# Optimization experiments

Hardware: AMD Instinct MI355X
Metric: run time of the kernel (lower is better)

The kernel has to match this reference:

```python
import jax, jax.numpy as jnp
import numpy as np

IMG = 800.0
OUT_H = OUT_W = 7
SR = 2  # sampling_ratio
SCALES = (0.25, 0.125, 0.0625, 0.03125)
CANON_SCALE = 224.0
CANON_LVL = 4.0
K_MIN, K_MAX = 2, 5


def _make_boxes(key, n):
    k1, k2, k3 = jax.random.split(key, 3)
    c = jax.random.uniform(k1, (n, 2), minval=0.0, maxval=IMG)          # centers (cx, cy)
    logs = jax.random.uniform(k2, (n, 2), minval=np.log(32.0), maxval=np.log(512.0))
    wh = jnp.exp(logs)                                                   # sizes 32..512 px
    x1y1 = jnp.clip(c - wh / 2, 0.0, IMG - 2.0)
    x2y2 = jnp.clip(c + wh / 2, x1y1 + 1.0, IMG)
    return jnp.concatenate([x1y1, x2y2], axis=1)  # [n,4] xyxy


def setup_inputs() -> dict:
    key = jax.random.key(0)
    ks = jax.random.split(key, 6)
    return {
        "feat0": jax.random.normal(ks[0], (2, 256, 200, 200), jnp.float32),
        "feat1": jax.random.normal(ks[1], (2, 256, 100, 100), jnp.float32),
        "feat2": jax.random.normal(ks[2], (2, 256, 50, 50), jnp.float32),
        "feat3": jax.random.normal(ks[3], (2, 256, 25, 25), jnp.float32),
        "boxes0": _make_boxes(ks[4], 256),
        "boxes1": _make_boxes(ks[5], 256),
    }


def _roi_align(feat_bhwc, rois, scale):
    """torchvision roi_align (aligned=False). feat_bhwc: [B,H,W,C], rois: [R,5] (b,x1,y1,x2,y2)."""
    B, H, W, C = feat_bhwc.shape
    R = rois.shape[0]
    bidx = rois[:, 0].astype(jnp.int32)
    x1, y1, x2, y2 = (rois[:, i] * scale for i in (1, 2, 3, 4))
    roi_w = jnp.maximum(x2 - x1, 1.0)
    roi_h = jnp.maximum(y2 - y1, 1.0)
    bin_w = roi_w / OUT_W
    bin_h = roi_h / OUT_H
    # sample grid: (g + 0.5)/SR bins == bin_index + (sub + 0.5)/SR
    gy = (jnp.arange(OUT_H * SR, dtype=feat_bhwc.dtype) + 0.5) / SR
    gx = (jnp.arange(OUT_W * SR, dtype=feat_bhwc.dtype) + 0.5) / SR
    y = y1[:, None] + gy[None, :] * bin_h[:, None]  # [R, GY]
    x = x1[:, None] + gx[None, :] * bin_w[:, None]  # [R, GX]

    def prep(c, size):
        valid = ((c > -1.0) & (c < size)).astype(feat_bhwc.dtype)
        c = jnp.clip(c, 0.0)
        lo = jnp.minimum(jnp.floor(c).astype(jnp.int32), size - 1)
        hi = jnp.minimum(lo + 1, size - 1)
        frac = jnp.where(lo >= size - 1, 0.0, c - lo.astype(feat_bhwc.dtype))
        return lo, hi, frac, valid

    yl, yh, fy, vy = prep(y, H)
    xl, xh, fx, vx = prep(x, W)
    b = bidx[:, None, None]

    def g(yi, xi):  # gather -> [R, GY, GX, C]
        return feat_bhwc[b, yi[:, :, None], xi[:, None, :]]

    wy = fy[:, :, None, None]
    wx = fx[:, None, :, None]
    val = (g(yl, xl) * (1 - wy) * (1 - wx) + g(yl, xh) * (1 - wy) * wx
           + g(yh, xl) * wy * (1 - wx) + g(yh, xh) * wy * wx)
    val = val * (vy[:, :, None, None] * vx[:, None, :, None])
    val = val.reshape(R, OUT_H, SR, OUT_W, SR, C).mean(axis=(2, 4))  # avg over SRxSR samples
    return jnp.transpose(val, (0, 3, 1, 2))  # [R, C, OUT_H, OUT_W]


def _forward(feat0, feat1, feat2, feat3, boxes0, boxes1):
    feats = [feat0, feat1, feat2, feat3]
    boxes = [boxes0, boxes1]
    # convert_to_roi_format
    ids = jnp.concatenate([jnp.full((b.shape[0], 1), i, dtype=b.dtype) for i, b in enumerate(boxes)], 0)
    cat = jnp.concatenate(boxes, 0)  # [R,4]
    rois = jnp.concatenate([ids, cat], 1)  # [R,5]
    # LevelMapper (FPN eq. 1)
    area = (cat[:, 2] - cat[:, 0]) * (cat[:, 3] - cat[:, 1])
    s = jnp.sqrt(area)
    tgt = jnp.floor(CANON_LVL + jnp.log2(s / CANON_SCALE) + 1e-6)
    levels = (jnp.clip(tgt, K_MIN, K_MAX) - K_MIN).astype(jnp.int32)  # [R] in 0..3
    per = [_roi_align(jnp.transpose(f, (0, 2, 3, 1)), rois, sc) for f, sc in zip(feats, SCALES)]
    stacked = jnp.stack(per)  # [L, R, C, 7, 7]
    R = rois.shape[0]
    return stacked[levels, jnp.arange(R)]  # route each roi to its level


def reference(feat0, feat1, feat2, feat3, boxes0, boxes1):
    return _forward(feat0, feat1, feat2, feat3, boxes0, boxes1)
```

## Files before the change

kernel.cpp:

```cpp
#include <hip/hip_runtime.h>


#define OUT_HW 7
#define NBINS 49
#define NCH 256
#define RPB 256

__global__ __launch_bounds__(256) void msroi_kernel(
    const float* __restrict__ f0, const float* __restrict__ f1,
    const float* __restrict__ f2, const float* __restrict__ f3,
    const float* __restrict__ boxes0, const float* __restrict__ boxes1,
    float* __restrict__ out)
{
    __shared__ float lds_out[NCH * NBINS];

    const int r    = blockIdx.x;
    const int tid  = threadIdx.x;
    const int lane = tid & 63;
    const int wid  = tid >> 6;

    const int b = (r < RPB) ? 0 : 1;
    const float* bx = (b == 0) ? (boxes0 + (size_t)r * 4)
                               : (boxes1 + (size_t)(r - RPB) * 4);
    const float x1b = bx[0], y1b = bx[1], x2b = bx[2], y2b = bx[3];

    const float area = (x2b - x1b) * (y2b - y1b);
    const float s    = sqrtf(area);
    const float tgt  = floorf(4.0f + log2f(s / 224.0f) + 1e-6f);
    const float lvlf = fminf(fmaxf(tgt, 2.0f), 5.0f);
    const int   lvl  = (int)lvlf - 2;

    int H, W;
    const float* feat;
    float scale;
    switch (lvl) {
      case 0:  feat = f0; H = 200; W = 200; scale = 0.25f;    break;
      case 1:  feat = f1; H = 100; W = 100; scale = 0.125f;   break;
      case 2:  feat = f2; H = 50;  W = 50;  scale = 0.0625f;  break;
      default: feat = f3; H = 25;  W = 25;  scale = 0.03125f; break;
    }
    const int HW = H * W;

    const float x1 = x1b * scale, y1 = y1b * scale;
    const float x2 = x2b * scale, y2 = y2b * scale;
    const float roi_w = fmaxf(x2 - x1, 1.0f);
    const float roi_h = fmaxf(y2 - y1, 1.0f);
    const float bin_w = roi_w / 7.0f;
    const float bin_h = roi_h / 7.0f;

    const bool active = (lane < NBINS);
    const int  binid  = active ? lane : 0;
    const int  oh = binid / 7, ow = binid % 7;

    int   offs[16];
    float wts[16];
    {
      int t = 0;
      #pragma unroll
      for (int sy = 0; sy < 2; ++sy) {
        const float iy = (float)(oh * 2 + sy);
        const float yy = y1 + ((iy + 0.5f) * 0.5f) * bin_h;
        const float vy = (yy > -1.0f && yy < (float)H) ? 1.0f : 0.0f;
        const float yc = fmaxf(yy, 0.0f);
        const int   yl = min((int)yc, H - 1);
        const int   yh = min(yl + 1, H - 1);
        const float fy = (yl >= H - 1) ? 0.0f : (yc - (float)yl);
        const float ay0 = vy * (1.0f - fy), ay1 = vy * fy;
        #pragma unroll
        for (int sx = 0; sx < 2; ++sx) {
          const float ix = (float)(ow * 2 + sx);
          const float xx = x1 + ((ix + 0.5f) * 0.5f) * bin_w;
          const float vx = (xx > -1.0f && xx < (float)W) ? 1.0f : 0.0f;
          const float xc = fmaxf(xx, 0.0f);
          const int   xl = min((int)xc, W - 1);
          const int   xh = min(xl + 1, W - 1);
          const float fx = (xl >= W - 1) ? 0.0f : (xc - (float)xl);
          const float ax0 = vx * (1.0f - fx), ax1 = vx * fx;
          offs[t] = yl * W + xl;  wts[t] = ay0 * ax0;  ++t;
          offs[t] = yl * W + xh;  wts[t] = ay0 * ax1;  ++t;
          offs[t] = yh * W + xl;  wts[t] = ay1 * ax0;  ++t;
          offs[t] = yh * W + xh;  wts[t] = ay1 * ax1;  ++t;
        }
      }
      if (!active) {
        #pragma unroll
        for (int k = 0; k < 16; ++k) { offs[k] = 0; wts[k] = 0.0f; }
      }
    }

    const float* fb = feat + (size_t)b * NCH * HW + (size_t)wid * 64 * HW;
    for (int ci = 0; ci < 64; ++ci) {
      const float* fc = fb + (size_t)ci * HW;
      float acc = 0.0f;
      #pragma unroll
      for (int k = 0; k < 16; ++k)
        acc += wts[k] * fc[offs[k]];
      if (active)
        lds_out[(wid * 64 + ci) * NBINS + binid] = acc * 0.25f;
    }

    __syncthreads();

    const size_t obase = (size_t)r * (NCH * NBINS);
    #pragma unroll 4
    for (int i = tid; i < NCH * NBINS; i += 256)
      out[obase + i] = lds_out[i];
}

extern "C" void kernel_launch(void* const* d_in, const int* in_sizes, int n_in,
                              void* d_out, int out_size, void* d_ws, size_t ws_size,
                              hipStream_t stream) {
    const float* f0 = (const float*)d_in[0];
    const float* f1 = (const float*)d_in[1];
    const float* f2 = (const float*)d_in[2];
    const float* f3 = (const float*)d_in[3];
    const float* b0 = (const float*)d_in[4];
    const float* b1 = (const float*)d_in[5];
    float* out = (float*)d_out;

    msroi_kernel<<<dim3(512), dim3(256), 0, stream>>>(f0, f1, f2, f3, b0, b1, out);
}
```

Baseline: 223.6 us.

## Transpose FPN features to NHWC in workspace and gather channel-contiguous float4s

Adds per-level transpose kernels that rewrite all four NCHW feature maps into NHWC in the workspace. A new ROI kernel then reads channel-contiguous float4 vectors per sample point, so accesses are coalesced instead of scattered per channel, and each ROI is split across two blocks by bins. The cost is a full read and write of about 109 MB of feature data on every call, plus extra launches. The old kernel is kept as a fallback when the workspace is too small.

```diff
diff --git a/kernel.cpp b/kernel.cpp
--- a/kernel.cpp
+++ b/kernel.cpp
@@ -1,38 +1,164 @@
 #include <hip/hip_runtime.h>
 
 
-#define OUT_HW 7
 #define NBINS 49
 #define NCH 256
 #define RPB 256
 
-__global__ __launch_bounds__(256) void msroi_kernel(
+#define OFS0 0
+#define OFS1 20480000
+#define OFS2 25600000
+#define OFS3 26880000
+#define WS_FLOATS 27200000
+
+__global__ __launch_bounds__(256) void transpose_kernel(
+    const float* __restrict__ src, float* __restrict__ dst, int HW)
+{
+    __shared__ float tile[64 * 65];
+    const int tid  = threadIdx.x;
+    const int lane = tid & 63;
+    const int wid  = tid >> 6;
+    const int hw0  = blockIdx.x * 64;
+    const int c0   = blockIdx.y * 64;
+    const int b    = blockIdx.z;
+
+    const float* sp = src + ((size_t)b * NCH + c0) * HW + hw0;
+    const bool inb = (hw0 + lane) < HW;
+    #pragma unroll
+    for (int i = 0; i < 16; ++i) {
+        const int cl = wid * 16 + i;
+        float v = 0.0f;
+        if (inb) v = sp[(size_t)cl * HW + lane];
+        tile[cl * 65 + lane] = v;
+    }
+    __syncthreads();
+    float* dp = dst + ((size_t)b * HW + hw0) * NCH + c0;
+    #pragma unroll
+    for (int k = 0; k < 16; ++k) {
+        const int hl = wid * 16 + k;
+        if (hw0 + hl < HW)
+            dp[(size_t)hl * NCH + lane] = tile[lane * 65 + hl];
+    }
+}
+
+__global__ __launch_bounds__(256) void roi_nhwc_kernel(
+    const float* __restrict__ ws,
+    const float* __restrict__ boxes0, const float* __restrict__ boxes1,
+    float* __restrict__ out)
+{
+    __shared__ float lds_out[25 * 257];
+
+    const int r    = blockIdx.x;
+    const int half = blockIdx.y;
+    const int tid  = threadIdx.x;
+    const int lane = tid & 63;
+    const int wid  = tid >> 6;
+
+    const int b = (r < RPB) ? 0 : 1;
+    const float* bx = (b == 0) ? (boxes0 + (size_t)r * 4)
+                               : (boxes1 + (size_t)(r - RPB) * 4);
+    const float x1b = bx[0], y1b = bx[1], x2b = bx[2], y2b = bx[3];
+
+    const float area = (x2b - x1b) * (y2b - y1b);
+    const float s    = sqrtf(area);
+    const float tgt  = floorf(4.0f + log2f(s / 224.0f) + 1e-6f);
+    const float lvlf = fminf(fmaxf(tgt, 2.0f), 5.0f);
+    const int   lvl  = (int)lvlf - 2;
+
+    int H, W; size_t base; float scale;
+    switch (lvl) {
+      case 0:  base = OFS0; H = 200; W = 200; scale = 0.25f;    break;
+      case 1:  base = OFS1; H = 100; W = 100; scale = 0.125f;   break;
+      case 2:  base = OFS2; H = 50;  W = 50;  scale = 0.0625f;  break;
+      default: base = OFS3; H = 25;  W = 25;  scale = 0.03125f; break;
+    }
+
+    const float x1 = x1b * scale, y1 = y1b * scale;
+    const float x2 = x2b * scale, y2 = y2b * scale;
+    const float roi_w = fmaxf(x2 - x1, 1.0f);
+    const float roi_h = fmaxf(y2 - y1, 1.0f);
+    const float bin_w = roi_w / 7.0f;
+    const float bin_h = roi_h / 7.0f;
+
+    const float* fb = ws + base + (size_t)b * H * W * NCH;
+    const int lc = 4 * lane;
+
+    const int bin0 = half * 25;
+    const int nb   = half ? 24 : 25;
+
+    for (int bi = wid; bi < nb; bi += 4) {
+        const int bin = bin0 + bi;
+        const int oh = bin / 7, ow = bin % 7;
+        float a0 = 0.0f, a1 = 0.0f, a2 = 0.0f, a3 = 0.0f;
+
+        #pragma unroll
+        for (int sy = 0; sy < 2; ++sy) {
+            const float yy = y1 + ((float)(oh * 2 + sy) + 0.5f) * 0.5f * bin_h;
+            const float vy = (yy > -1.0f && yy < (float)H) ? 1.0f : 0.0f;
+            const float yc = fmaxf(yy, 0.0f);
+            const int   yl = min((int)yc, H - 1);
+            const int   yh = min(yl + 1, H - 1);
+            const float fy = (yl >= H - 1) ? 0.0f : (yc - (float)yl);
+            #pragma unroll
+            for (int sx = 0; sx < 2; ++sx) {
+                const float xx = x1 + ((float)(ow * 2 + sx) + 0.5f) * 0.5f * bin_w;
+                const float vx = (xx > -1.0f && xx < (float)W) ? 1.0f : 0.0f;
+                const float xc = fmaxf(xx, 0.0f);
+                const int   xl = min((int)xc, W - 1);
+                const int   xh = min(xl + 1, W - 1);
+                const float fx = (xl >= W - 1) ? 0.0f : (xc - (float)xl);
+                const float vv  = vy * vx * 0.25f;
+                const float w00 = vv * (1.0f - fy) * (1.0f - fx);
+                const float w01 = vv * (1.0f - fy) * fx;
+                const float w10 = vv * fy * (1.0f - fx);
+                const float w11 = vv * fy * fx;
+
+                const float4 v00 = *(const float4*)(fb + ((size_t)(yl * W + xl)) * NCH + lc);
+                const float4 v01 = *(const float4*)(fb + ((size_t)(yl * W + xh)) * NCH + lc);
+                const float4 v10 = *(const float4*)(fb + ((size_t)(yh * W + xl)) * NCH + lc);
+                const float4 v11 = *(const float4*)(fb + ((size_t)(yh * W + xh)) * NCH + lc);
+
+                a0 += w00 * v00.x + w01 * v01.x + w10 * v10.x + w11 * v11.x;
+                a1 += w00 * v00.y + w01 * v01.y + w10 * v10.y + w11 * v11.y;
+                a2 += w00 * v00.z + w01 * v01.z + w10 * v10.z + w11 * v11.z;
+                a3 += w00 * v00.w + w01 * v01.w + w10 * v10.w + w11 * v11.w;
+            }
+        }
+        const int lb = bi * 257 + lc;
+        lds_out[lb + 0] = a0;
+        lds_out[lb + 1] = a1;
+        lds_out[lb + 2] = a2;
+        lds_out[lb + 3] = a3;
+    }
+
+    __syncthreads();
+
+    const size_t obase = (size_t)r * (NCH * NBINS) + bin0;
+    for (int i = tid; i < NCH * nb; i += 256) {
+        const int c  = i / nb;
+        const int bj = i - c * nb;
+        out[obase + (size_t)c * NBINS + bj] = lds_out[bj * 257 + c];
+    }
+}
+
+__global__ __launch_bounds__(256) void msroi_fallback(
     const float* __restrict__ f0, const float* __restrict__ f1,
     const float* __restrict__ f2, const float* __restrict__ f3,
     const float* __restrict__ boxes0, const float* __restrict__ boxes1,
     float* __restrict__ out)
 {
     __shared__ float lds_out[NCH * NBINS];
-
-    const int r    = blockIdx.x;
-    const int tid  = threadIdx.x;
-    const int lane = tid & 63;
-    const int wid  = tid >> 6;
-
+    const int r = blockIdx.x, tid = threadIdx.x;
+    const int lane = tid & 63, wid = tid >> 6;
     const int b = (r < RPB) ? 0 : 1;
     const float* bx = (b == 0) ? (boxes0 + (size_t)r * 4)
                                : (boxes1 + (size_t)(r - RPB) * 4);
     const float x1b = bx[0], y1b = bx[1], x2b = bx[2], y2b = bx[3];
-
     const float area = (x2b - x1b) * (y2b - y1b);
-    const float s    = sqrtf(area);
-    const float tgt  = floorf(4.0f + log2f(s / 224.0f) + 1e-6f);
-    const float lvlf = fminf(fmaxf(tgt, 2.0f), 5.0f);
-    const int   lvl  = (int)lvlf - 2;
-
-    int H, W;
-    const float* feat;
-    float scale;
+    const float s = sqrtf(area);
+    const float tgt = floorf(4.0f + log2f(s / 224.0f) + 1e-6f);
+    const int lvl = (int)fminf(fmaxf(tgt, 2.0f), 5.0f) - 2;
+    int H, W; const float* feat; float scale;
     switch (lvl) {
       case 0:  feat = f0; H = 200; W = 200; scale = 0.25f;    break;
       case 1:  feat = f1; H = 100; W = 100; scale = 0.125f;   break;
@@ -40,46 +166,38 @@
       default: feat = f3; H = 25;  W = 25;  scale = 0.03125f; break;
     }
     const int HW = H * W;
-
     const float x1 = x1b * scale, y1 = y1b * scale;
     const float x2 = x2b * scale, y2 = y2b * scale;
-    const float roi_w = fmaxf(x2 - x1, 1.0f);
-    const float roi_h = fmaxf(y2 - y1, 1.0f);
-    const float bin_w = roi_w / 7.0f;
-    const float bin_h = roi_h / 7.0f;
-
+    const float roi_w = fmaxf(x2 - x1, 1.0f), roi_h = fmaxf(y2 - y1, 1.0f);
+    const float bin_w = roi_w / 7.0f, bin_h = roi_h / 7.0f;
     const bool active = (lane < NBINS);
-    const int  binid  = active ? lane : 0;
-    const int  oh = binid / 7, ow = binid % 7;
-
-    int   offs[16];
-    float wts[16];
+    const int binid = active ? lane : 0;
+    const int oh = binid / 7, ow = binid % 7;
+    int offs[16]; float wts[16];
     {
       int t = 0;
       #pragma unroll
       for (int sy = 0; sy < 2; ++sy) {
-        const float iy = (float)(oh * 2 + sy);
-        const float yy = y1 + ((iy + 0.5f) * 0.5f) * bin_h;
+        const float yy = y1 + ((float)(oh * 2 + sy) + 0.5f) * 0.5f * bin_h;
         const float vy = (yy > -1.0f && yy < (float)H) ? 1.0f : 0.0f;
         const float yc = fmaxf(yy, 0.0f);
-        const int   yl = min((int)yc, H - 1);
-        const int   yh = min(yl + 1, H - 1);
+        const int yl = min((int)yc, H - 1);
+        const int yh = min(yl + 1, H - 1);
         const float fy = (yl >= H - 1) ? 0.0f : (yc - (float)yl);
         const float ay0 = vy * (1.0f - fy), ay1 = vy * fy;
         #pragma unroll
         for (int sx = 0; sx < 2; ++sx) {
-          const float ix = (float)(ow * 2 + sx);
-          const float xx = x1 + ((ix + 0.5f) * 0.5f) * bin_w;
+          const float xx = x1 + ((float)(ow * 2 + sx) + 0.5f) * 0.5f * bin_w;
           const float vx = (xx > -1.0f && xx < (float)W) ? 1.0f : 0.0f;
           const float xc = fmaxf(xx, 0.0f);
-          const int   xl = min((int)xc, W - 1);
-          const int   xh = min(xl + 1, W - 1);
+          const int xl = min((int)xc, W - 1);
+          const int xh = min(xl + 1, W - 1);
           const float fx = (xl >= W - 1) ? 0.0f : (xc - (float)xl);
           const float ax0 = vx * (1.0f - fx), ax1 = vx * fx;
-          offs[t] = yl * W + xl;  wts[t] = ay0 * ax0;  ++t;
-          offs[t] = yl * W + xh;  wts[t] = ay0 * ax1;  ++t;
-          offs[t] = yh * W + xl;  wts[t] = ay1 * ax0;  ++t;
-          offs[t] = yh * W + xh;  wts[t] = ay1 * ax1;  ++t;
+          offs[t] = yl * W + xl; wts[t] = ay0 * ax0; ++t;
+          offs[t] = yl * W + xh; wts[t] = ay0 * ax1; ++t;
+          offs[t] = yh * W + xl; wts[t] = ay1 * ax0; ++t;
+          offs[t] = yh * W + xh; wts[t] = ay1 * ax1; ++t;
         }
       }
       if (!active) {
@@ -87,24 +205,18 @@
         for (int k = 0; k < 16; ++k) { offs[k] = 0; wts[k] = 0.0f; }
       }
     }
-
-    const float* fb = feat + (size_t)b * NCH * HW + (size_t)wid * 64 * HW;
+    const float* fbb = feat + (size_t)b * NCH * HW + (size_t)wid * 64 * HW;
     for (int ci = 0; ci < 64; ++ci) {
-      const float* fc = fb + (size_t)ci * HW;
+      const float* fc = fbb + (size_t)ci * HW;
       float acc = 0.0f;
       #pragma unroll
-      for (int k = 0; k < 16; ++k)
-        acc += wts[k] * fc[offs[k]];
-      if (active)
-        lds_out[(wid * 64 + ci) * NBINS + binid] = acc * 0.25f;
-    }
-
+      for (int k = 0; k < 16; ++k) acc += wts[k] * fc[offs[k]];
+      if (active) lds_out[(wid * 64 + ci) * NBINS + binid] = acc * 0.25f;
+    }
     __syncthreads();
-
     const size_t obase = (size_t)r * (NCH * NBINS);
     #pragma unroll 4
-    for (int i = tid; i < NCH * NBINS; i += 256)
-      out[obase + i] = lds_out[i];
+    for (int i = tid; i < NCH * NBINS; i += 256) out[obase + i] = lds_out[i];
 }
 
 extern "C" void kernel_launch(void* const* d_in, const int* in_sizes, int n_in,
@@ -117,6 +229,15 @@
     const float* b0 = (const float*)d_in[4];
     const float* b1 = (const float*)d_in[5];
     float* out = (float*)d_out;
-
-    msroi_kernel<<<dim3(512), dim3(256), 0, stream>>>(f0, f1, f2, f3, b0, b1, out);
-}
+    float* ws  = (float*)d_ws;
+
+    if (ws_size >= (size_t)WS_FLOATS * 4) {
+        transpose_kernel<<<dim3(625, 4, 2), 256, 0, stream>>>(f0, ws + OFS0, 40000);
+        transpose_kernel<<<dim3(157, 4, 2), 256, 0, stream>>>(f1, ws + OFS1, 10000);
+        transpose_kernel<<<dim3(40,  4, 2), 256, 0, stream>>>(f2, ws + OFS2, 2500);
+        transpose_kernel<<<dim3(10,  4, 2), 256, 0, stream>>>(f3, ws + OFS3, 625);
+        roi_nhwc_kernel<<<dim3(512, 2), 256, 0, stream>>>(ws, b0, b1, out);
+    } else {
+        msroi_fallback<<<dim3(512), 256, 0, stream>>>(f0, f1, f2, f3, b0, b1, out);
+    }
+}
```

Measured after the change: 247.3 us. +10.6%, slower.
